# Performance work log

Hardware: AMD Instinct MI355X
Metric: run time of the kernel (lower is better)

## Reference

```python
import jax, jax.numpy as jnp
import numpy as np

B, N, D = 8, 4096, 256
H = W = 64          # grid_size = img_size // patch_size = 256 // 4
WS = 8              # swin window size
NH = 8              # swin heads
M = 16              # fno modes
E = 4               # num experts
TD = 768            # text dim
HID = 1024          # mlp hidden = 4 * D
TK = 2              # top_k


def gelu(x):
    return jax.nn.gelu(x, approximate=False)


def layernorm(x, g, b, eps=1e-5):
    mu = x.mean(-1, keepdims=True)
    var = ((x - mu) ** 2).mean(-1, keepdims=True)
    return (x - mu) * jax.lax.rsqrt(var + eps) * g + b


def fno_expert(x, w1r, w1i, w2r, w2i, conv_w, conv_b):
    # x: [B, N, D] -> grid [B, D, H, W]
    xg = x.transpose(0, 2, 1).reshape(B, D, H, W)
    xft = jnp.fft.rfft2(xg)                      # [B, D, H, W//2+1] complex64
    w1 = w1r + 1j * w1i
    w2 = w2r + 1j * w2i
    top = jnp.einsum('bixy,ioxy->boxy', xft[:, :, :M, :M], w1)
    bot = jnp.einsum('bixy,ioxy->boxy', xft[:, :, -M:, :M], w2)
    out_ft = jnp.zeros((B, D, H, W // 2 + 1), dtype=xft.dtype)
    out_ft = out_ft.at[:, :, :M, :M].set(top).at[:, :, -M:, :M].set(bot)
    x1 = jnp.fft.irfft2(out_ft, s=(H, W))        # [B, D, H, W]
    x2 = jnp.einsum('bdhw,do->bohw', xg, conv_w) + conv_b[None, :, None, None]
    out = gelu(x1 + x2)
    return out.reshape(B, D, N).transpose(0, 2, 1) + x


def mlp_expert(x, w1, b1, w2, b2):
    return gelu(x @ w1 + b1) @ w2 + b2 + x


def window_attn_expert(x, ln1_g, ln1_b, qkv_w, qkv_b, out_w, out_b,
                       ln2_g, ln2_b, mw1, mb1, mw2, mb2):
    shortcut = x
    h = layernorm(x, ln1_g, ln1_b)
    # window partition: [B,H,W,C] -> [B*nW, WS*WS, C]
    h = h.reshape(B, H // WS, WS, W // WS, WS, D)
    h = h.transpose(0, 1, 3, 2, 4, 5).reshape(-1, WS * WS, D)
    # multi-head self attention (torch nn.MultiheadAttention semantics)
    qkv = h @ qkv_w + qkv_b                      # [Bw, L, 3D]
    q, k, v = jnp.split(qkv, 3, axis=-1)
    dh = D // NH
    def heads(t):
        return t.reshape(-1, WS * WS, NH, dh).transpose(0, 2, 1, 3)
    q, k, v = heads(q), heads(k), heads(v)
    scores = jnp.einsum('whld,whmd->whlm', q, k) / jnp.sqrt(jnp.float32(dh))
    attn = jax.nn.softmax(scores, axis=-1)
    o = jnp.einsum('whlm,whmd->whld', attn, v)
    o = o.transpose(0, 2, 1, 3).reshape(-1, WS * WS, D)
    o = o @ out_w + out_b
    # window reverse
    o = o.reshape(B, H // WS, W // WS, WS, WS, D)
    o = o.transpose(0, 1, 3, 2, 4, 5).reshape(B, N, D)
    x = o + shortcut
    h2 = layernorm(x, ln2_g, ln2_b)
    return x + (gelu(h2 @ mw1 + mb1) @ mw2 + mb2)


def setup_inputs() -> dict:
    key = jax.random.key(0)
    ks = jax.random.split(key, 24)
    rn = lambda k, s: jax.random.normal(k, s, jnp.float32) * 0.02
    fscale = 1.0 / (D * D)
    ru = lambda k: jax.random.uniform(k, (D, D, M, M), jnp.float32) * fscale
    return {
        'x': jax.random.normal(ks[0], (B, N, D), jnp.float32),
        'text_embedding': jax.random.normal(ks[1], (B, TD), jnp.float32),
        'gate_w1': rn(ks[2], (D + TD, D)), 'gate_b1': jnp.zeros((D,), jnp.float32),
        'gate_w2': rn(ks[3], (D, E)), 'gate_b2': jnp.zeros((E,), jnp.float32),
        'fno_w1r': ru(ks[4]), 'fno_w1i': ru(ks[5]),
        'fno_w2r': ru(ks[6]), 'fno_w2i': ru(ks[7]),
        'fno_conv_w': rn(ks[8], (D, D)), 'fno_conv_b': jnp.zeros((D,), jnp.float32),
        'mlp1_w1': rn(ks[9], (D, HID)), 'mlp1_b1': jnp.zeros((HID,), jnp.float32),
        'mlp1_w2': rn(ks[10], (HID, D)), 'mlp1_b2': jnp.zeros((D,), jnp.float32),
        'mlp2_w1': rn(ks[11], (D, HID)), 'mlp2_b1': jnp.zeros((HID,), jnp.float32),
        'mlp2_w2': rn(ks[12], (HID, D)), 'mlp2_b2': jnp.zeros((D,), jnp.float32),
        'wa_ln1_g': jnp.ones((D,), jnp.float32), 'wa_ln1_b': jnp.zeros((D,), jnp.float32),
        'wa_qkv_w': rn(ks[13], (D, 3 * D)), 'wa_qkv_b': jnp.zeros((3 * D,), jnp.float32),
        'wa_out_w': rn(ks[14], (D, D)), 'wa_out_b': jnp.zeros((D,), jnp.float32),
        'wa_ln2_g': jnp.ones((D,), jnp.float32), 'wa_ln2_b': jnp.zeros((D,), jnp.float32),
        'wa_mlp_w1': rn(ks[15], (D, HID)), 'wa_mlp_b1': jnp.zeros((HID,), jnp.float32),
        'wa_mlp_w2': rn(ks[16], (HID, D)), 'wa_mlp_b2': jnp.zeros((D,), jnp.float32),
    }


def reference(x, text_embedding, gate_w1, gate_b1, gate_w2, gate_b2,
              fno_w1r, fno_w1i, fno_w2r, fno_w2i, fno_conv_w, fno_conv_b,
              mlp1_w1, mlp1_b1, mlp1_w2, mlp1_b2,
              mlp2_w1, mlp2_b1, mlp2_w2, mlp2_b2,
              wa_ln1_g, wa_ln1_b, wa_qkv_w, wa_qkv_b, wa_out_w, wa_out_b,
              wa_ln2_g, wa_ln2_b, wa_mlp_w1, wa_mlp_b1, wa_mlp_w2, wa_mlp_b2):
    # --- gating ---
    feat = jnp.concatenate([x.mean(axis=1), text_embedding], axis=1)  # [B, D+TD]
    logits = jax.nn.relu(feat @ gate_w1 + gate_b1) @ gate_w2 + gate_b2  # [B, E]
    top_v, top_i = jax.lax.top_k(logits, TK)
    weights = jax.nn.softmax(top_v, axis=-1)                           # [B, TK]
    # per-expert combined weight: cw[b,e] = sum_k w[b,k] * (idx[b,k]==e)
    cw = (jax.nn.one_hot(top_i, E, dtype=x.dtype) * weights[..., None]).sum(axis=1)  # [B, E]
    # --- experts (FNO, MLP, WindowAttn, MLP) ---
    e0 = fno_expert(x, fno_w1r, fno_w1i, fno_w2r, fno_w2i, fno_conv_w, fno_conv_b)
    e1 = mlp_expert(x, mlp1_w1, mlp1_b1, mlp1_w2, mlp1_b2)
    e2 = window_attn_expert(x, wa_ln1_g, wa_ln1_b, wa_qkv_w, wa_qkv_b,
                            wa_out_w, wa_out_b, wa_ln2_g, wa_ln2_b,
                            wa_mlp_w1, wa_mlp_b1, wa_mlp_w2, wa_mlp_b2)
    e3 = mlp_expert(x, mlp2_w1, mlp2_b1, mlp2_w2, mlp2_b2)
    outs = jnp.stack([e0, e1, e2, e3])                                 # [E, B, N, D]
    final = jnp.einsum('be,ebnd->bnd', cw, outs)
    return final, weights
```

## Files before the change

### kernel.cpp

```cpp
#include <hip/hip_runtime.h>
#include <math.h>


#define NB 8
#define NN 4096
#define DD 256

typedef __attribute__((ext_vector_type(8))) short bf16x8;
typedef __attribute__((ext_vector_type(4))) float f32x4;

__device__ __forceinline__ float gelu_f(float v) {
    return 0.5f * v * (1.0f + erff(v * 0.7071067811865475f));
}
__device__ __forceinline__ ushort f2bf(float f) {
    uint32_t u = __float_as_uint(f);
    uint32_t r = (u + 0x7fffu + ((u >> 16) & 1u)) >> 16;
    return (ushort)r;
}
__device__ __forceinline__ float b2f(ushort h) {
    return __uint_as_float(((uint32_t)h) << 16);
}

__global__ void k_gate_mean1(const float* __restrict__ x, float* __restrict__ partial) {
    int c = blockIdx.x, b = blockIdx.y;
    int t = threadIdx.x;
    const float* xb = x + ((size_t)b * NN + c * 128) * DD;
    float s = 0.f;
    for (int n = 0; n < 128; ++n) s += xb[(size_t)n * DD + t];
    partial[((size_t)b * 32 + c) * 256 + t] = s;
}
__global__ void k_gate_mean2(const float* __restrict__ partial, const float* __restrict__ text,
                             float* __restrict__ feat) {
    int b = blockIdx.x, t = threadIdx.x;
    float s = 0.f;
    for (int c = 0; c < 32; ++c) s += partial[((size_t)b * 32 + c) * 256 + t];
    feat[b * 1024 + t] = s * (1.0f / NN);
    for (int j = t; j < 768; j += 256) feat[b * 1024 + 256 + j] = text[b * 768 + j];
}

__global__ void k_gate_mlp1(const float* __restrict__ feat, const float* __restrict__ w1,
                            const float* __restrict__ b1, float* __restrict__ h1) {
    int b = blockIdx.x, j = threadIdx.x;
    float acc = b1[j];
    const float* f = feat + b * 1024;
    for (int k = 0; k < 1024; ++k) acc += f[k] * w1[k * 256 + j];
    h1[b * 256 + j] = fmaxf(acc, 0.f);
}

__global__ void k_gate_top(const float* __restrict__ h1, const float* __restrict__ w2,
                           const float* __restrict__ b2, float* __restrict__ cw,
                           float* __restrict__ wout) {
    __shared__ float lg[8][4];
    int t = threadIdx.x;
    if (t < 32) {
        int b = t >> 2, e = t & 3;
        float acc = b2[e];
        const float* h = h1 + b * 256;
        for (int k = 0; k < 256; ++k) acc += h[k] * w2[k * 4 + e];
        lg[b][e] = acc;
    }
    __syncthreads();
    if (t < 8) {
        int b = t;
        float v[4];
        #pragma unroll
        for (int e = 0; e < 4; ++e) v[e] = lg[b][e];
        int i0 = 0;
        #pragma unroll
        for (int e = 1; e < 4; ++e) if (v[e] > v[i0]) i0 = e;
        int i1 = -1;
        #pragma unroll
        for (int e = 0; e < 4; ++e) {
            if (e == i0) continue;
            if (i1 < 0 || v[e] > v[i1]) i1 = e;
        }
        float v0 = v[i0], v1 = v[i1];
        float e1v = expf(v1 - v0);
        float inv = 1.0f / (1.0f + e1v);
        float w0 = inv, w1v = e1v * inv;
        wout[b * 2 + 0] = w0;
        wout[b * 2 + 1] = w1v;
        float c[4] = {0.f, 0.f, 0.f, 0.f};
        c[i0] += w0; c[i1] += w1v;
        #pragma unroll
        for (int e = 0; e < 4; ++e) cw[b * 4 + e] = c[e];
    }
}

__global__ void k_cvtbf(const float* __restrict__ src, ushort* __restrict__ dst) {
    int i = blockIdx.x * 256 + threadIdx.x;
    float4 v = ((const float4*)src)[i];
    ushort4 o;
    o.x = f2bf(v.x); o.y = f2bf(v.y); o.z = f2bf(v.z); o.w = f2bf(v.w);
    ((ushort4*)dst)[i] = o;
}

__global__ void k_wt(const float* __restrict__ src, ushort* __restrict__ dst, int K, int N) {
    __shared__ float tile[32][33];
    int n0 = blockIdx.x * 32, k0 = blockIdx.y * 32;
    int tx = threadIdx.x, ty = threadIdx.y;
    #pragma unroll
    for (int i = 0; i < 4; ++i)
        tile[ty + i * 8][tx] = src[(size_t)(k0 + ty + i * 8) * N + n0 + tx];
    __syncthreads();
    #pragma unroll
    for (int i = 0; i < 4; ++i)
        dst[(size_t)(n0 + ty + i * 8) * K + k0 + tx] = f2bf(tile[tx][ty + i * 8]);
}

template<int MODE>
__global__ void __launch_bounds__(256) k_gemm(const ushort* __restrict__ A,
        const ushort* __restrict__ Bt, const float* __restrict__ bias,
        const float* __restrict__ res, float* __restrict__ outf,
        ushort* __restrict__ outb, const float* __restrict__ cw, int eidx,
        int K, int Ncols, size_t bsA, size_t bsB, size_t bsC) {
    __shared__ alignas(16) char smem[32768];
    ushort* sA = (ushort*)smem;
    ushort* sB = (ushort*)(smem + 16384);
    int z = blockIdx.z;
    A += z * bsA; Bt += z * bsB;
    if (outf) outf += z * bsC;
    if (outb) outb += z * bsC;
    int m0 = blockIdx.x * 128;
    int n0 = blockIdx.y * 128;
    int t = threadIdx.x;
    int lane = t & 63, wid = t >> 6;
    int wr = wid >> 1, wc = wid & 1;
    int rlo = lane & 15, khi = (lane >> 4) * 8;

    auto stage = [&](int buf, int k0) {
        const ushort* Ab = A + (size_t)m0 * K + k0;
        const ushort* Bb = Bt + (size_t)n0 * K + k0;
        #pragma unroll
        for (int h = 0; h < 2; ++h) {
            int s = t + h * 256;
            int row = s >> 2, kc = (s & 3) * 8;
            __builtin_amdgcn_global_load_lds(
                (const __attribute__((address_space(1))) void*)(Ab + (size_t)row * K + kc),
                (__attribute__((address_space(3))) void*)(sA + buf * 4096 + s * 8),
                16, 0, 0);
            __builtin_amdgcn_global_load_lds(
                (const __attribute__((address_space(1))) void*)(Bb + (size_t)row * K + kc),
                (__attribute__((address_space(3))) void*)(sB + buf * 4096 + s * 8),
                16, 0, 0);
        }
    };

    f32x4 acc[4][4];
    #pragma unroll
    for (int i = 0; i < 4; ++i)
        #pragma unroll
        for (int j = 0; j < 4; ++j) acc[i][j] = (f32x4){0.f, 0.f, 0.f, 0.f};

    int KT = K >> 5;
    stage(0, 0);
    int cur = 0;
    for (int kt = 0; kt < KT; ++kt) {
        __syncthreads();
        if (kt + 1 < KT) stage(cur ^ 1, (kt + 1) << 5);
        const ushort* Ap = sA + cur * 4096;
        const ushort* Bp = sB + cur * 4096;
        bf16x8 af[4], bfr[4];
        #pragma unroll
        for (int i = 0; i < 4; ++i) {
            af[i]  = *(const bf16x8*)(Ap + (wr * 64 + i * 16 + rlo) * 32 + khi);
            bfr[i] = *(const bf16x8*)(Bp + (wc * 64 + i * 16 + rlo) * 32 + khi);
        }
        #pragma unroll
        for (int i = 0; i < 4; ++i)
            #pragma unroll
            for (int j = 0; j < 4; ++j)
                acc[i][j] = __builtin_amdgcn_mfma_f32_16x16x32_bf16(af[i], bfr[j], acc[i][j], 0, 0, 0);
        cur ^= 1;
    }

    float bj4[4];
    if constexpr (MODE != 4 && MODE != 5) {
        #pragma unroll
        for (int nt = 0; nt < 4; ++nt) bj4[nt] = bias[n0 + wc * 64 + nt * 16 + rlo];
    }

    if constexpr (MODE == 0 || MODE == 1 || MODE == 5) {
        ushort* eb = (ushort*)smem;
        #pragma unroll
        for (int mt = 0; mt < 4; ++mt) {
            __syncthreads();
            #pragma unroll
            for (int nt = 0; nt < 4; ++nt) {
                int col = wc * 64 + nt * 16 + rlo;
                #pragma unroll
                for (int j = 0; j < 4; ++j) {
                    float v = acc[mt][nt][j];
                    if constexpr (MODE == 5)
                        v += bias[m0 + wr * 64 + mt * 16 + (lane >> 4) * 4 + j];
                    else
                        v += bj4[nt];
                    if (MODE == 0) v = gelu_f(v);
                    eb[(wr * 16 + (lane >> 4) * 4 + j) * 136 + col] = f2bf(v);
                }
            }
            __syncthreads();
            #pragma unroll
            for (int h = 0; h < 2; ++h) {
                int s = t + h * 256;
                int r = s >> 4, c = (s & 15) * 8;
                int grow = m0 + (r >> 4) * 64 + mt * 16 + (r & 15);
                *(uint4*)(outb + (size_t)grow * Ncols + n0 + c) = *(uint4*)&eb[r * 136 + c];
            }
        }
    } else {
        float* ep = (float*)smem;
        #pragma unroll
        for (int mt = 0; mt < 4; ++mt) {
            __syncthreads();
            #pragma unroll
            for (int nt = 0; nt < 4; ++nt) {
                int col = wc * 64 + nt * 16 + rlo;
                #pragma unroll
                for (int j = 0; j < 4; ++j) {
                    float v = acc[mt][nt][j];
                    if constexpr (MODE == 4)
                        v += bias[m0 + wr * 64 + mt * 16 + (lane >> 4) * 4 + j];
                    else
                        v += bj4[nt];
                    ep[(wr * 16 + (lane >> 4) * 4 + j) * 132 + col] = v;
                }
            }
            __syncthreads();
            #pragma unroll
            for (int h = 0; h < 4; ++h) {
                int s = t + h * 256;
                int r = s >> 5, c4 = (s & 31) * 4;
                int grow = m0 + (r >> 4) * 64 + mt * 16 + (r & 15);
                size_t g = (size_t)grow * Ncols + n0 + c4;
                float4 v = *(float4*)&ep[r * 132 + c4];
                if constexpr (MODE == 2) {
                    if (res) {
                        float4 rv = *(const float4*)&res[g];
                        v.x += rv.x; v.y += rv.y; v.z += rv.z; v.w += rv.w;
                    }
                    *(float4*)&outf[g] = v;
                } else if constexpr (MODE == 4) {
                    *(float4*)&outf[g] = v;
                } else {
                    float cwv = cw[(grow >> 12) * 4 + eidx];
                    float4 rv = *(const float4*)&res[g];
                    float4 ov = *(float4*)&outf[g];
                    ov.x += cwv * (v.x + rv.x);
                    ov.y += cwv * (v.y + rv.y);
                    ov.z += cwv * (v.z + rv.z);
                    ov.w += cwv * (v.w + rv.w);
                    *(float4*)&outf[g] = ov;
                }
            }
        }
    }
}

__global__ void k_transpose(const float* __restrict__ x, float* __restrict__ xg) {
    __shared__ float tile[32][33];
    int b = blockIdx.z;
    int nt = blockIdx.x, dt = blockIdx.y;
    int tx = threadIdx.x, ty = threadIdx.y;
    const float* xb = x + (size_t)b * NN * DD;
    float* xgb = xg + (size_t)b * DD * NN;
    #pragma unroll
    for (int i = 0; i < 4; ++i) {
        int n = nt * 32 + ty + i * 8;
        tile[ty + i * 8][tx] = xb[(size_t)n * DD + dt * 32 + tx];
    }
    __syncthreads();
    #pragma unroll
    for (int i = 0; i < 4; ++i) {
        int d = dt * 32 + ty + i * 8;
        xgb[(size_t)d * NN + nt * 32 + tx] = tile[tx][ty + i * 8];
    }
}

__global__ void __launch_bounds__(64) k_rfft2(const float* __restrict__ xg, float* __restrict__ xft) {
    __shared__ float plane[64][65];
    __shared__ float s1[64][16][2];
    __shared__ float twc[64], tws[64];
    int p = blockIdx.x;
    int t = threadIdx.x;
    const float* src = xg + (size_t)p * 4096;
    for (int i = 0; i < 64; ++i) plane[i][t] = src[i * 64 + t];
    twc[t] = cosf((float)t * (6.283185307179586f / 64.0f));
    tws[t] = sinf((float)t * (6.283185307179586f / 64.0f));
    __syncthreads();
    int r = t;
    for (int kw = 0; kw < 16; ++kw) {
        float re = 0.f, im = 0.f;
        for (int w = 0; w < 64; ++w) {
            int j = (w * kw) & 63;
            float xv = plane[r][w];
            re += xv * twc[j];
            im -= xv * tws[j];
        }
        s1[r][kw][0] = re; s1[r][kw][1] = im;
    }
    __syncthreads();
    float2* dst = (float2*)xft + (size_t)p * 512;
    #pragma unroll
    for (int q = 0; q < 8; ++q) {
        int oi = t + q * 64;
        int krow = oi >> 4, kw = oi & 15;
        int kh = krow < 16 ? krow : krow + 32;
        float re = 0.f, im = 0.f;
        for (int h = 0; h < 64; ++h) {
            int j = (h * kh) & 63;
            float c = twc[j], s = tws[j];
            float ar = s1[h][kw][0], ai = s1[h][kw][1];
            re += ar * c + ai * s;
            im += ai * c - ar * s;
        }
        dst[oi] = make_float2(re, im);
    }
}

__global__ void __launch_bounds__(512) k_spectral(const float* __restrict__ xft,
        const float* __restrict__ w1r, const float* __restrict__ w1i,
        const float* __restrict__ w2r, const float* __restrict__ w2i,
        float* __restrict__ part) {
    __shared__ alignas(16) ushort Wl[32 * 648];
    __shared__ alignas(16) ushort Xl[16 * 648];
    int z = blockIdx.z;
    int region = z >> 1, is = z & 1;
    const float* wrp = region ? w2r : w1r;
    const float* wip = region ? w2i : w1i;
    int xm = blockIdx.y;
    int krow = region * 16 + xm;
    int o0 = blockIdx.x * 16;
    int t = threadIdx.x;
    int wv = t >> 6, lane = t & 63;
    int rlo = lane & 15, khi = lane >> 4;
    int ibase = is * 128;

    f32x4 acc[2][2];
    #pragma unroll
    for (int a = 0; a < 2; ++a)
        #pragma unroll
        for (int b = 0; b < 2; ++b) acc[a][b] = (f32x4){0.f, 0.f, 0.f, 0.f};

    for (int ch = 0; ch < 4; ++ch) {
        int i0 = ibase + ch * 32;
        __syncthreads();
        #pragma unroll
        for (int s = 0; s < 2; ++s) {
            int m = t + s * 512;
            int y4 = m & 3, ol = (m >> 2) & 15, i8 = (m >> 6) & 7, arr = m >> 9;
            const float* wsrc = arr ? wip : wrp;
            int ig = i0 + i8 * 4;
            float4 f[4];
            #pragma unroll
            for (int u = 0; u < 4; ++u)
                f[u] = *(const float4*)&wsrc[((size_t)(ig + u) * 256 + o0 + ol) * 256 + xm * 16 + y4 * 4];
            #pragma unroll
            for (int yy2 = 0; yy2 < 4; ++yy2) {
                int y = y4 * 4 + yy2;
                ushort4 pk;
                pk.x = f2bf(((const float*)&f[0])[yy2]);
                pk.y = f2bf(((const float*)&f[1])[yy2]);
                pk.z = f2bf(((const float*)&f[2])[yy2]);
                pk.w = f2bf(((const float*)&f[3])[yy2]);
                *(ushort4*)&Wl[(y * 2 + arr) * 648 + ol * 40 + i8 * 4] = pk;
            }
        }
        #pragma unroll
        for (int s = 0; s < 2; ++s) {
            int m = t + s * 512;
            int y = m & 15, i4 = (m >> 4) & 7, b = (m >> 7) & 7;
            int ig = i0 + i4 * 4;
            float2 g[4];
            #pragma unroll
            for (int u = 0; u < 4; ++u)
                g[u] = *(const float2*)&xft[(((size_t)(b * 256 + ig + u)) * 32 + krow) * 32 + y * 2];
            ushort4 re, im;
            re.x = f2bf(g[0].x); re.y = f2bf(g[1].x); re.z = f2bf(g[2].x); re.w = f2bf(g[3].x);
            im.x = f2bf(g[0].y); im.y = f2bf(g[1].y); im.z = f2bf(g[2].y); im.w = f2bf(g[3].y);
            *(ushort4*)&Xl[b * 648 + y * 40 + i4 * 4] = re;
            *(ushort4*)&Xl[(b + 8) * 648 + y * 40 + i4 * 4] = im;
        }
        __syncthreads();
        #pragma unroll
        for (int yy = 0; yy < 2; ++yy) {
            int y = wv * 2 + yy;
            bf16x8 Bf = *(const bf16x8*)&Xl[rlo * 648 + y * 40 + khi * 8];
            #pragma unroll
            for (int arr = 0; arr < 2; ++arr) {
                bf16x8 Af = *(const bf16x8*)&Wl[(y * 2 + arr) * 648 + rlo * 40 + khi * 8];
                acc[yy][arr] = __builtin_amdgcn_mfma_f32_16x16x32_bf16(Af, Bf, acc[yy][arr], 0, 0, 0);
            }
        }
    }

    float* dp = part + (size_t)is * 4194304;
    int c = rlo;
    int b = c & 7, hi = c >> 3;
    #pragma unroll
    for (int yy = 0; yy < 2; ++yy) {
        int y = wv * 2 + yy;
        #pragma unroll
        for (int j = 0; j < 4; ++j) {
            float C1 = acc[yy][0][j];
            float c2x = __shfl_xor(acc[yy][1][j], 8);
            float val = hi ? (c2x + C1) : (C1 - c2x);
            int o = o0 + khi * 4 + j;
            dp[(((size_t)(b * 256 + o) * 32 + krow) * 16 + y) * 2 + hi] = val;
        }
    }
}

__global__ void __launch_bounds__(64) k_irfft_fuse(const float* __restrict__ part,
        const ushort* __restrict__ x2t, ushort* __restrict__ tmp) {
    __shared__ float F[32][16][2];
    __shared__ float tarr[64][16][2];
    __shared__ float twc[64], tws[64];
    int p = blockIdx.x;
    int t = threadIdx.x;
    const float2* s0 = (const float2*)part + (size_t)p * 512;
    #pragma unroll
    for (int l = 0; l < 8; ++l) {
        int idx = t + l * 64;
        float2 a = s0[idx];
        float2 b2 = s0[idx + 2097152];
        ((float2*)F)[idx] = make_float2(a.x + b2.x, a.y + b2.y);
    }
    twc[t] = cosf((float)t * (6.283185307179586f / 64.0f));
    tws[t] = sinf((float)t * (6.283185307179586f / 64.0f));
    __syncthreads();
    int h = t;
    for (int kw = 0; kw < 16; ++kw) {
        float re = 0.f, im = 0.f;
        #pragma unroll
        for (int krow = 0; krow < 32; ++krow) {
            int kh = krow < 16 ? krow : krow + 32;
            int j = (h * kh) & 63;
            float c = twc[j], s = tws[j];
            float fr = F[krow][kw][0], fi = F[krow][kw][1];
            re += fr * c - fi * s;
            im += fr * s + fi * c;
        }
        tarr[h][kw][0] = re * (1.f / 64.f);
        tarr[h][kw][1] = im * (1.f / 64.f);
    }
    __syncthreads();
    const ushort* x2p = x2t + (size_t)p * 4096;
    ushort* tp = tmp + (size_t)p * 4096;
    for (int q = 0; q < 64; ++q) {
        int w = t;
        float acc = tarr[q][0][0];
        #pragma unroll
        for (int kw = 1; kw < 16; ++kw) {
            int j = (w * kw) & 63;
            acc += 2.f * (tarr[q][kw][0] * twc[j] - tarr[q][kw][1] * tws[j]);
        }
        float x1 = acc * (1.f / 64.f);
        int idx = q * 64 + w;
        tp[idx] = f2bf(gelu_f(x1 + b2f(x2p[idx])));
    }
}

__global__ void k_fno_final(const ushort* __restrict__ tmp, const float* __restrict__ x,
        const float* __restrict__ cw, float* __restrict__ out) {
    __shared__ float tile[32][33];
    int b = blockIdx.z;
    int n0 = blockIdx.x * 32, d0 = blockIdx.y * 32;
    int tx = threadIdx.x, ty = threadIdx.y;
    const ushort* tb = tmp + (size_t)b * DD * NN;
    #pragma unroll
    for (int i = 0; i < 4; ++i)
        tile[ty + i * 8][tx] = b2f(tb[(size_t)(d0 + ty + i * 8) * NN + n0 + tx]);
    __syncthreads();
    float cw0 = cw[b * 4];
    #pragma unroll
    for (int i = 0; i < 4; ++i) {
        int n = n0 + ty + i * 8, d = d0 + tx;
        size_t g = ((size_t)b * NN + n) * DD + d;
        out[g] = cw0 * (tile[tx][ty + i * 8] + x[g]);
    }
}

__global__ void __launch_bounds__(256) k_ln(const float* __restrict__ in, const float* __restrict__ g,
        const float* __restrict__ be, ushort* __restrict__ outb) {
    int row = blockIdx.x * 4 + (threadIdx.x >> 6);
    int lane = threadIdx.x & 63;
    const float4* rp = (const float4*)(in + (size_t)row * 256);
    float4 v = rp[lane];
    float s = v.x + v.y + v.z + v.w;
    float s2 = v.x * v.x + v.y * v.y + v.z * v.z + v.w * v.w;
    #pragma unroll
    for (int off = 32; off > 0; off >>= 1) {
        s += __shfl_down(s, off);
        s2 += __shfl_down(s2, off);
    }
    s = __shfl(s, 0); s2 = __shfl(s2, 0);
    float mu = s * (1.f / 256.f);
    float var = s2 * (1.f / 256.f) - mu * mu;
    float rstd = rsqrtf(var + 1e-5f);
    float4 gv = ((const float4*)g)[lane];
    float4 bv = ((const float4*)be)[lane];
    ushort4 ov;
    ov.x = f2bf((v.x - mu) * rstd * gv.x + bv.x);
    ov.y = f2bf((v.y - mu) * rstd * gv.y + bv.y);
    ov.z = f2bf((v.z - mu) * rstd * gv.z + bv.z);
    ov.w = f2bf((v.w - mu) * rstd * gv.w + bv.w);
    ((ushort4*)(outb + (size_t)row * 256))[lane] = ov;
}

__global__ void __launch_bounds__(256) k_window_attn(const ushort* __restrict__ qkvb,
        ushort* __restrict__ aob) {
    __shared__ ushort lds[4 * 7424];
    int t = threadIdx.x;
    int w = t >> 6, lane = t & 63;
    int wi = blockIdx.x, hh = blockIdx.y;
    int hd = hh * 4 + w;
    int b = wi >> 6, hb = (wi >> 3) & 7, wb = wi & 7;
    ushort* A = lds + w * 7424;
    ushort* Kl = A + 2560;
    ushort* Vt = A + 5120;
    int rlo = lane & 15, kq = lane >> 4;

    int tok = lane;
    int n = hb * 512 + wb * 8 + ((tok >> 3) << 6) + (tok & 7);
    const ushort* gq = qkvb + ((size_t)b * 4096 + n) * 768 + hd * 32;
    const uint4* qp = (const uint4*)gq;
    const uint4* kp = (const uint4*)(gq + 256);
    const uint4* vp = (const uint4*)(gq + 512);
    uint4 q0 = qp[0], q1 = qp[1], q2 = qp[2], q3 = qp[3];
    uint4 k0 = kp[0], k1 = kp[1], k2 = kp[2], k3 = kp[3];
    uint4 v0 = vp[0], v1 = vp[1], v2 = vp[2], v3 = vp[3];
    uint4* qr = (uint4*)(A + tok * 40);
    qr[0] = q0; qr[1] = q1; qr[2] = q2; qr[3] = q3;
    uint4* kr = (uint4*)(Kl + tok * 40);
    kr[0] = k0; kr[1] = k1; kr[2] = k2; kr[3] = k3;
    ushort vbuf[32];
    *(uint4*)&vbuf[0] = v0; *(uint4*)&vbuf[8] = v1;
    *(uint4*)&vbuf[16] = v2; *(uint4*)&vbuf[24] = v3;
    #pragma unroll
    for (int d = 0; d < 32; ++d) Vt[d * 72 + tok] = vbuf[d];
    __syncthreads();

    bf16x8 Qf[4], Kf[4];
    #pragma unroll
    for (int lt = 0; lt < 4; ++lt)
        Qf[lt] = *(const bf16x8*)(A + (lt * 16 + rlo) * 40 + kq * 8);
    #pragma unroll
    for (int mt = 0; mt < 4; ++mt)
        Kf[mt] = *(const bf16x8*)(Kl + (mt * 16 + rlo) * 40 + kq * 8);

    f32x4 S[4][4];
    #pragma unroll
    for (int lt = 0; lt < 4; ++lt)
        #pragma unroll
        for (int mt = 0; mt < 4; ++mt)
            S[lt][mt] = __builtin_amdgcn_mfma_f32_16x16x32_bf16(Qf[lt], Kf[mt],
                        (f32x4){0.f, 0.f, 0.f, 0.f}, 0, 0, 0);
    __syncthreads();

    const float scale = 0.17677669529663687f;
    float inv_[4][4];
    #pragma unroll
    for (int lt = 0; lt < 4; ++lt) {
        float m4[4], s4[4];
        #pragma unroll
        for (int j = 0; j < 4; ++j) {
            m4[j] = fmaxf(fmaxf(S[lt][0][j], S[lt][1][j]), fmaxf(S[lt][2][j], S[lt][3][j]));
        }
        #pragma unroll
        for (int off = 1; off < 16; off <<= 1)
            #pragma unroll
            for (int j = 0; j < 4; ++j) m4[j] = fmaxf(m4[j], __shfl_xor(m4[j], off));
        #pragma unroll
        for (int j = 0; j < 4; ++j) s4[j] = 0.f;
        #pragma unroll
        for (int mt = 0; mt < 4; ++mt)
            #pragma unroll
            for (int j = 0; j < 4; ++j) {
                float p = expf((S[lt][mt][j] - m4[j]) * scale);
                s4[j] += p;
                A[(lt * 16 + kq * 4 + j) * 72 + mt * 16 + rlo] = f2bf(p);
            }
        #pragma unroll
        for (int off = 1; off < 16; off <<= 1)
            #pragma unroll
            for (int j = 0; j < 4; ++j) s4[j] += __shfl_xor(s4[j], off);
        #pragma unroll
        for (int j = 0; j < 4; ++j) inv_[lt][j] = 1.0f / s4[j];
    }
    __syncthreads();

    f32x4 O[4][2];
    #pragma unroll
    for (int lt = 0; lt < 4; ++lt)
        #pragma unroll
        for (int dt = 0; dt < 2; ++dt) {
            f32x4 o = (f32x4){0.f, 0.f, 0.f, 0.f};
            #pragma unroll
            for (int mc = 0; mc < 2; ++mc) {
                bf16x8 pa = *(const bf16x8*)(A + (lt * 16 + rlo) * 72 + mc * 32 + kq * 8);
                bf16x8 vb = *(const bf16x8*)(Vt + (dt * 16 + rlo) * 72 + mc * 32 + kq * 8);
                o = __builtin_amdgcn_mfma_f32_16x16x32_bf16(pa, vb, o, 0, 0, 0);
            }
            O[lt][dt] = o;
        }
    __syncthreads();

    #pragma unroll
    for (int lt = 0; lt < 4; ++lt)
        #pragma unroll
        for (int dt = 0; dt < 2; ++dt)
            #pragma unroll
            for (int j = 0; j < 4; ++j)
                A[(lt * 16 + kq * 4 + j) * 40 + dt * 16 + rlo] = f2bf(O[lt][dt][j] * inv_[lt][j]);
    __syncthreads();
    const uint4* orow = (const uint4*)(A + lane * 40);
    uint4 o0 = orow[0], o1 = orow[1], o2 = orow[2], o3 = orow[3];
    uint4* gout = (uint4*)(aob + ((size_t)b * 4096 + n) * 256 + hd * 32);
    gout[0] = o0; gout[1] = o1; gout[2] = o2; gout[3] = o3;
}

extern "C" void kernel_launch(void* const* d_in, const int* in_sizes, int n_in,
                              void* d_out, int out_size, void* d_ws, size_t ws_size,
                              hipStream_t stream) {
    (void)in_sizes; (void)n_in; (void)out_size; (void)ws_size;
    const float* x        = (const float*)d_in[0];
    const float* text     = (const float*)d_in[1];
    const float* gate_w1  = (const float*)d_in[2];
    const float* gate_b1  = (const float*)d_in[3];
    const float* gate_w2  = (const float*)d_in[4];
    const float* gate_b2  = (const float*)d_in[5];
    const float* fno_w1r  = (const float*)d_in[6];
    const float* fno_w1i  = (const float*)d_in[7];
    const float* fno_w2r  = (const float*)d_in[8];
    const float* fno_w2i  = (const float*)d_in[9];
    const float* fno_cw   = (const float*)d_in[10];
    const float* fno_cb   = (const float*)d_in[11];
    const float* mlp1_w1  = (const float*)d_in[12];
    const float* mlp1_b1  = (const float*)d_in[13];
    const float* mlp1_w2  = (const float*)d_in[14];
    const float* mlp1_b2  = (const float*)d_in[15];
    const float* mlp2_w1  = (const float*)d_in[16];
    const float* mlp2_b1  = (const float*)d_in[17];
    const float* mlp2_w2  = (const float*)d_in[18];
    const float* mlp2_b2  = (const float*)d_in[19];
    const float* ln1_g    = (const float*)d_in[20];
    const float* ln1_b    = (const float*)d_in[21];
    const float* qkv_w    = (const float*)d_in[22];
    const float* qkv_b    = (const float*)d_in[23];
    const float* out_w    = (const float*)d_in[24];
    const float* out_b    = (const float*)d_in[25];
    const float* ln2_g    = (const float*)d_in[26];
    const float* ln2_b    = (const float*)d_in[27];
    const float* wa_w1    = (const float*)d_in[28];
    const float* wa_b1    = (const float*)d_in[29];
    const float* wa_w2    = (const float*)d_in[30];
    const float* wa_b2    = (const float*)d_in[31];

    float* ws   = (float*)d_ws;
    float* feat = ws;
    float* h1   = ws + 8192;
    float* cwp  = ws + 10240;
    ushort* wbf = (ushort*)(ws + 16384);
    ushort* w1aT = wbf;
    ushort* w2aT = w1aT + 262144;
    ushort* w1bT = w2aT + 262144;
    ushort* w2bT = w1bT + 262144;
    ushort* w1cT = w2bT + 262144;
    ushort* w2cT = w1cT + 262144;
    ushort* qkvT = w2cT + 262144;
    ushort* outwT = qkvT + 196608;
    ushort* convT = outwT + 65536;
    ushort* Xbf  = (ushort*)(ws + 16384 + 1048576);
    float* slotA = ws + 16384 + 1048576 + 4194304;
    ushort* abf  = (ushort*)slotA;
    float* xft   = slotA + 8388608;
    float* oft   = xft + 2097152;
    float* regD  = oft + 2097152;
    ushort* bigb = (ushort*)(regD + 8388608);
    float* gpart = oft;

    float* outp = (float*)d_out;
    float* wout = outp + (size_t)NB * NN * DD;

    k_gate_mean1<<<dim3(32, 8), 256, 0, stream>>>(x, gpart);
    k_gate_mean2<<<8, 256, 0, stream>>>(gpart, text, feat);
    k_gate_mlp1<<<8, 256, 0, stream>>>(feat, gate_w1, gate_b1, h1);
    k_gate_top<<<1, 64, 0, stream>>>(h1, gate_w2, gate_b2, cwp, wout);

    k_cvtbf<<<8192, 256, 0, stream>>>(x, Xbf);
    dim3 wtb(32, 8);
    k_wt<<<dim3(32, 8), wtb, 0, stream>>>(mlp1_w1, w1aT, 256, 1024);
    k_wt<<<dim3(8, 32), wtb, 0, stream>>>(mlp1_w2, w2aT, 1024, 256);
    k_wt<<<dim3(32, 8), wtb, 0, stream>>>(mlp2_w1, w1bT, 256, 1024);
    k_wt<<<dim3(8, 32), wtb, 0, stream>>>(mlp2_w2, w2bT, 1024, 256);
    k_wt<<<dim3(32, 8), wtb, 0, stream>>>(wa_w1, w1cT, 256, 1024);
    k_wt<<<dim3(8, 32), wtb, 0, stream>>>(wa_w2, w2cT, 1024, 256);
    k_wt<<<dim3(24, 8), wtb, 0, stream>>>(qkv_w, qkvT, 256, 768);
    k_wt<<<dim3(8, 8), wtb, 0, stream>>>(out_w, outwT, 256, 256);
    k_wt<<<dim3(8, 8), wtb, 0, stream>>>(fno_cw, convT, 256, 256);

    k_transpose<<<dim3(128, 8, 8), dim3(32, 8), 0, stream>>>(x, slotA);
    k_rfft2<<<2048, 64, 0, stream>>>(slotA, xft);
    k_gemm<5><<<dim3(2, 32, 8), 256, 0, stream>>>(convT, Xbf, fno_cb, nullptr, nullptr,
        (ushort*)regD, nullptr, 0, 256, 4096, 0, (size_t)NN * DD, (size_t)DD * NN);
    k_spectral<<<dim3(16, 16, 4), 512, 0, stream>>>(xft, fno_w1r, fno_w1i, fno_w2r, fno_w2i, slotA);
    k_irfft_fuse<<<2048, 64, 0, stream>>>(slotA, (const ushort*)regD, bigb);
    k_fno_final<<<dim3(128, 8, 8), dim3(32, 8), 0, stream>>>(bigb, x, cwp, outp);

    k_gemm<0><<<dim3(256, 8), 256, 0, stream>>>(Xbf, w1aT, mlp1_b1, nullptr, nullptr, bigb, nullptr, 0, 256, 1024, 0, 0, 0);
    k_gemm<3><<<dim3(256, 2), 256, 0, stream>>>(bigb, w2aT, mlp1_b2, x, outp, nullptr, cwp, 1, 1024, 256, 0, 0, 0);

    k_ln<<<8192, 256, 0, stream>>>(x, ln1_g, ln1_b, abf);
    k_gemm<1><<<dim3(256, 6), 256, 0, stream>>>(abf, qkvT, qkv_b, nullptr, nullptr, bigb, nullptr, 0, 256, 768, 0, 0, 0);
    k_window_attn<<<dim3(512, 2), 256, 0, stream>>>(bigb, abf);
    k_gemm<2><<<dim3(256, 2), 256, 0, stream>>>(abf, outwT, out_b, x, regD, nullptr, nullptr, 0, 256, 256, 0, 0, 0);
    k_ln<<<8192, 256, 0, stream>>>(regD, ln2_g, ln2_b, abf);
    k_gemm<0><<<dim3(256, 8), 256, 0, stream>>>(abf, w1cT, wa_b1, nullptr, nullptr, bigb, nullptr, 0, 256, 1024, 0, 0, 0);
    k_gemm<3><<<dim3(256, 2), 256, 0, stream>>>(bigb, w2cT, wa_b2, regD, outp, nullptr, cwp, 2, 1024, 256, 0, 0, 0);

    k_gemm<0><<<dim3(256, 8), 256, 0, stream>>>(Xbf, w1bT, mlp2_b1, nullptr, nullptr, bigb, nullptr, 0, 256, 1024, 0, 0, 0);
    k_gemm<3><<<dim3(256, 2), 256, 0, stream>>>(bigb, w2bT, mlp2_b2, x, outp, nullptr, cwp, 3, 1024, 256, 0, 0, 0);
}
```

Baseline: 694.9 us.

## Widen FFT blocks to 256 threads and split spectral kernel over y halves

The rfft2 and irfft fusion kernels now run 256 threads per plane instead of 64. The frequency loops are split across four thread groups, and the shared intermediate buffers change to a padded transposed layout to reduce bank conflicts. The spectral mixing kernel splits the mode-y dimension into two halves across the grid, which doubles the block count and halves shared memory per block, so each wave does one y instead of two. This targets low occupancy and long serial loops in the FNO path, at the cost of more blocks and reloading the input tiles for each half.

```diff
diff --git a/kernel.cpp b/kernel.cpp
--- a/kernel.cpp
+++ b/kernel.cpp
@@ -277,19 +277,28 @@
     }
 }
 
-__global__ void __launch_bounds__(64) k_rfft2(const float* __restrict__ xg, float* __restrict__ xft) {
+__global__ void __launch_bounds__(256) k_rfft2(const float* __restrict__ xg, float* __restrict__ xft) {
     __shared__ float plane[64][65];
-    __shared__ float s1[64][16][2];
+    __shared__ float s1re[16][66], s1im[16][66];
     __shared__ float twc[64], tws[64];
     int p = blockIdx.x;
     int t = threadIdx.x;
+    int tx = t & 63, grp = t >> 6;
     const float* src = xg + (size_t)p * 4096;
-    for (int i = 0; i < 64; ++i) plane[i][t] = src[i * 64 + t];
-    twc[t] = cosf((float)t * (6.283185307179586f / 64.0f));
-    tws[t] = sinf((float)t * (6.283185307179586f / 64.0f));
-    __syncthreads();
-    int r = t;
-    for (int kw = 0; kw < 16; ++kw) {
+    #pragma unroll
+    for (int i = 0; i < 16; ++i) {
+        int row = grp * 16 + i;
+        plane[row][tx] = src[row * 64 + tx];
+    }
+    if (t < 64) {
+        twc[t] = cosf((float)t * (6.283185307179586f / 64.0f));
+        tws[t] = sinf((float)t * (6.283185307179586f / 64.0f));
+    }
+    __syncthreads();
+    int r = tx;
+    #pragma unroll
+    for (int q = 0; q < 4; ++q) {
+        int kw = grp + q * 4;
         float re = 0.f, im = 0.f;
         for (int w = 0; w < 64; ++w) {
             int j = (w * kw) & 63;
@@ -297,20 +306,21 @@
             re += xv * twc[j];
             im -= xv * tws[j];
         }
-        s1[r][kw][0] = re; s1[r][kw][1] = im;
+        s1re[kw][r] = re;
+        s1im[kw][r] = im;
     }
     __syncthreads();
     float2* dst = (float2*)xft + (size_t)p * 512;
     #pragma unroll
-    for (int q = 0; q < 8; ++q) {
-        int oi = t + q * 64;
+    for (int q = 0; q < 2; ++q) {
+        int oi = t + q * 256;
         int krow = oi >> 4, kw = oi & 15;
         int kh = krow < 16 ? krow : krow + 32;
         float re = 0.f, im = 0.f;
         for (int h = 0; h < 64; ++h) {
             int j = (h * kh) & 63;
             float c = twc[j], s = tws[j];
-            float ar = s1[h][kw][0], ai = s1[h][kw][1];
+            float ar = s1re[kw][h], ai = s1im[kw][h];
             re += ar * c + ai * s;
             im += ai * c - ar * s;
         }
@@ -322,10 +332,10 @@
         const float* __restrict__ w1r, const float* __restrict__ w1i,
         const float* __restrict__ w2r, const float* __restrict__ w2i,
         float* __restrict__ part) {
-    __shared__ alignas(16) ushort Wl[32 * 648];
-    __shared__ alignas(16) ushort Xl[16 * 648];
+    __shared__ alignas(16) ushort Wl[16 * 648];
+    __shared__ alignas(16) ushort Xl[16 * 328];
     int z = blockIdx.z;
-    int region = z >> 1, is = z & 1;
+    int region = z >> 2, is = (z >> 1) & 1, yh = z & 1;
     const float* wrp = region ? w2r : w1r;
     const float* wip = region ? w2i : w1i;
     int xm = blockIdx.y;
@@ -336,101 +346,92 @@
     int rlo = lane & 15, khi = lane >> 4;
     int ibase = is * 128;
 
-    f32x4 acc[2][2];
-    #pragma unroll
-    for (int a = 0; a < 2; ++a)
-        #pragma unroll
-        for (int b = 0; b < 2; ++b) acc[a][b] = (f32x4){0.f, 0.f, 0.f, 0.f};
+    int sy4 = t & 1, sol = (t >> 1) & 15, si8 = (t >> 5) & 7, sarr = (t >> 8) & 1;
+    const float* wsrc = sarr ? wip : wrp;
+    int xy = t & 7, xi4 = (t >> 3) & 7, xb = (t >> 6) & 7;
+
+    f32x4 acc[2];
+    acc[0] = (f32x4){0.f, 0.f, 0.f, 0.f};
+    acc[1] = (f32x4){0.f, 0.f, 0.f, 0.f};
 
     for (int ch = 0; ch < 4; ++ch) {
         int i0 = ibase + ch * 32;
         __syncthreads();
-        #pragma unroll
-        for (int s = 0; s < 2; ++s) {
-            int m = t + s * 512;
-            int y4 = m & 3, ol = (m >> 2) & 15, i8 = (m >> 6) & 7, arr = m >> 9;
-            const float* wsrc = arr ? wip : wrp;
-            int ig = i0 + i8 * 4;
+        {
+            int ig = i0 + si8 * 4;
             float4 f[4];
             #pragma unroll
             for (int u = 0; u < 4; ++u)
-                f[u] = *(const float4*)&wsrc[((size_t)(ig + u) * 256 + o0 + ol) * 256 + xm * 16 + y4 * 4];
+                f[u] = *(const float4*)&wsrc[((size_t)(ig + u) * 256 + o0 + sol) * 256 + xm * 16 + (yh * 2 + sy4) * 4];
             #pragma unroll
             for (int yy2 = 0; yy2 < 4; ++yy2) {
-                int y = y4 * 4 + yy2;
+                int yl = sy4 * 4 + yy2;
                 ushort4 pk;
                 pk.x = f2bf(((const float*)&f[0])[yy2]);
                 pk.y = f2bf(((const float*)&f[1])[yy2]);
                 pk.z = f2bf(((const float*)&f[2])[yy2]);
                 pk.w = f2bf(((const float*)&f[3])[yy2]);
-                *(ushort4*)&Wl[(y * 2 + arr) * 648 + ol * 40 + i8 * 4] = pk;
+                *(ushort4*)&Wl[(yl * 2 + sarr) * 648 + sol * 40 + si8 * 4] = pk;
             }
         }
-        #pragma unroll
-        for (int s = 0; s < 2; ++s) {
-            int m = t + s * 512;
-            int y = m & 15, i4 = (m >> 4) & 7, b = (m >> 7) & 7;
-            int ig = i0 + i4 * 4;
+        {
+            int ig = i0 + xi4 * 4;
             float2 g[4];
             #pragma unroll
             for (int u = 0; u < 4; ++u)
-                g[u] = *(const float2*)&xft[(((size_t)(b * 256 + ig + u)) * 32 + krow) * 32 + y * 2];
+                g[u] = *(const float2*)&xft[(((size_t)(xb * 256 + ig + u)) * 32 + krow) * 32 + (yh * 8 + xy) * 2];
             ushort4 re, im;
             re.x = f2bf(g[0].x); re.y = f2bf(g[1].x); re.z = f2bf(g[2].x); re.w = f2bf(g[3].x);
             im.x = f2bf(g[0].y); im.y = f2bf(g[1].y); im.z = f2bf(g[2].y); im.w = f2bf(g[3].y);
-            *(ushort4*)&Xl[b * 648 + y * 40 + i4 * 4] = re;
-            *(ushort4*)&Xl[(b + 8) * 648 + y * 40 + i4 * 4] = im;
+            *(ushort4*)&Xl[xb * 328 + xy * 40 + xi4 * 4] = re;
+            *(ushort4*)&Xl[(xb + 8) * 328 + xy * 40 + xi4 * 4] = im;
         }
         __syncthreads();
-        #pragma unroll
-        for (int yy = 0; yy < 2; ++yy) {
-            int y = wv * 2 + yy;
-            bf16x8 Bf = *(const bf16x8*)&Xl[rlo * 648 + y * 40 + khi * 8];
-            #pragma unroll
-            for (int arr = 0; arr < 2; ++arr) {
-                bf16x8 Af = *(const bf16x8*)&Wl[(y * 2 + arr) * 648 + rlo * 40 + khi * 8];
-                acc[yy][arr] = __builtin_amdgcn_mfma_f32_16x16x32_bf16(Af, Bf, acc[yy][arr], 0, 0, 0);
-            }
+        bf16x8 Bf = *(const bf16x8*)&Xl[rlo * 328 + wv * 40 + khi * 8];
+        #pragma unroll
+        for (int arr = 0; arr < 2; ++arr) {
+            bf16x8 Af = *(const bf16x8*)&Wl[(wv * 2 + arr) * 648 + rlo * 40 + khi * 8];
+            acc[arr] = __builtin_amdgcn_mfma_f32_16x16x32_bf16(Af, Bf, acc[arr], 0, 0, 0);
         }
     }
 
     float* dp = part + (size_t)is * 4194304;
-    int c = rlo;
-    int b = c & 7, hi = c >> 3;
-    #pragma unroll
-    for (int yy = 0; yy < 2; ++yy) {
-        int y = wv * 2 + yy;
-        #pragma unroll
-        for (int j = 0; j < 4; ++j) {
-            float C1 = acc[yy][0][j];
-            float c2x = __shfl_xor(acc[yy][1][j], 8);
-            float val = hi ? (c2x + C1) : (C1 - c2x);
-            int o = o0 + khi * 4 + j;
-            dp[(((size_t)(b * 256 + o) * 32 + krow) * 16 + y) * 2 + hi] = val;
-        }
-    }
-}
-
-__global__ void __launch_bounds__(64) k_irfft_fuse(const float* __restrict__ part,
+    int b = rlo & 7, hi = rlo >> 3;
+    int y = yh * 8 + wv;
+    #pragma unroll
+    for (int j = 0; j < 4; ++j) {
+        float C1 = acc[0][j];
+        float c2x = __shfl_xor(acc[1][j], 8);
+        float val = hi ? (c2x + C1) : (C1 - c2x);
+        int o = o0 + khi * 4 + j;
+        dp[(((size_t)(b * 256 + o) * 32 + krow) * 16 + y) * 2 + hi] = val;
+    }
+}
+
+__global__ void __launch_bounds__(256) k_irfft_fuse(const float* __restrict__ part,
         const ushort* __restrict__ x2t, ushort* __restrict__ tmp) {
     __shared__ float F[32][16][2];
-    __shared__ float tarr[64][16][2];
+    __shared__ float tre[16][66], tim[16][66];
     __shared__ float twc[64], tws[64];
     int p = blockIdx.x;
     int t = threadIdx.x;
     const float2* s0 = (const float2*)part + (size_t)p * 512;
     #pragma unroll
-    for (int l = 0; l < 8; ++l) {
-        int idx = t + l * 64;
+    for (int l = 0; l < 2; ++l) {
+        int idx = t + l * 256;
         float2 a = s0[idx];
         float2 b2 = s0[idx + 2097152];
         ((float2*)F)[idx] = make_float2(a.x + b2.x, a.y + b2.y);
     }
-    twc[t] = cosf((float)t * (6.283185307179586f / 64.0f));
-    tws[t] = sinf((float)t * (6.283185307179586f / 64.0f));
-    __syncthreads();
-    int h = t;
-    for (int kw = 0; kw < 16; ++kw) {
+    if (t < 64) {
+        twc[t] = cosf((float)t * (6.283185307179586f / 64.0f));
+        tws[t] = sinf((float)t * (6.283185307179586f / 64.0f));
+    }
+    __syncthreads();
+    int h = t & 63;
+    #pragma unroll
+    for (int q = 0; q < 4; ++q) {
+        int kw = (t >> 6) + q * 4;
         float re = 0.f, im = 0.f;
         #pragma unroll
         for (int krow = 0; krow < 32; ++krow) {
@@ -441,22 +442,24 @@
             re += fr * c - fi * s;
             im += fr * s + fi * c;
         }
-        tarr[h][kw][0] = re * (1.f / 64.f);
-        tarr[h][kw][1] = im * (1.f / 64.f);
+        tre[kw][h] = re * (1.f / 64.f);
+        tim[kw][h] = im * (1.f / 64.f);
     }
     __syncthreads();
     const ushort* x2p = x2t + (size_t)p * 4096;
     ushort* tp = tmp + (size_t)p * 4096;
-    for (int q = 0; q < 64; ++q) {
-        int w = t;
-        float acc = tarr[q][0][0];
+    int w = t & 63;
+    #pragma unroll
+    for (int qq = 0; qq < 16; ++qq) {
+        int qrow = (t >> 6) + qq * 4;
+        float acc = tre[0][qrow];
         #pragma unroll
         for (int kw = 1; kw < 16; ++kw) {
             int j = (w * kw) & 63;
-            acc += 2.f * (tarr[q][kw][0] * twc[j] - tarr[q][kw][1] * tws[j]);
+            acc += 2.f * (tre[kw][qrow] * twc[j] - tim[kw][qrow] * tws[j]);
         }
         float x1 = acc * (1.f / 64.f);
-        int idx = q * 64 + w;
+        int idx = qrow * 64 + w;
         tp[idx] = f2bf(gelu_f(x1 + b2f(x2p[idx])));
     }
 }
@@ -701,11 +704,11 @@
     k_wt<<<dim3(8, 8), wtb, 0, stream>>>(fno_cw, convT, 256, 256);
 
     k_transpose<<<dim3(128, 8, 8), dim3(32, 8), 0, stream>>>(x, slotA);
-    k_rfft2<<<2048, 64, 0, stream>>>(slotA, xft);
+    k_rfft2<<<2048, 256, 0, stream>>>(slotA, xft);
     k_gemm<5><<<dim3(2, 32, 8), 256, 0, stream>>>(convT, Xbf, fno_cb, nullptr, nullptr,
         (ushort*)regD, nullptr, 0, 256, 4096, 0, (size_t)NN * DD, (size_t)DD * NN);
-    k_spectral<<<dim3(16, 16, 4), 512, 0, stream>>>(xft, fno_w1r, fno_w1i, fno_w2r, fno_w2i, slotA);
-    k_irfft_fuse<<<2048, 64, 0, stream>>>(slotA, (const ushort*)regD, bigb);
+    k_spectral<<<dim3(16, 16, 8), 512, 0, stream>>>(xft, fno_w1r, fno_w1i, fno_w2r, fno_w2i, slotA);
+    k_irfft_fuse<<<2048, 256, 0, stream>>>(slotA, (const ushort*)regD, bigb);
     k_fno_final<<<dim3(128, 8, 8), dim3(32, 8), 0, stream>>>(bigb, x, cwp, outp);
 
     k_gemm<0><<<dim3(256, 8), 256, 0, stream>>>(Xbf, w1aT, mlp1_b1, nullptr, nullptr, bigb, nullptr, 0, 256, 1024, 0, 0, 0);
```

New measurement: 731.7 us. 1.05x slower.
